# Kernel optimization log

Hardware: AMD Instinct MI355X
Metric: run time of the kernel (lower is better)

The kernel has to match this reference:

```python
import jax, jax.numpy as jnp
import numpy as np

B, Cin, C, H, W = 2, 64, 128, 64, 64
D_INNER, N_STATE, DT_RANK, K = 256, 16, 8, 4


def _silu(x):
    return x * jax.nn.sigmoid(x)


def _layernorm(x, g, b, eps=1e-5):
    mu = x.mean(-1, keepdims=True)
    var = ((x - mu) ** 2).mean(-1, keepdims=True)
    return (x - mu) * jax.lax.rsqrt(var + eps) * g + b


def setup_inputs():
    key = jax.random.key(0)
    ks = jax.random.split(key, 16)
    f32 = jnp.float32
    inp = {}
    inp["x"] = jax.random.normal(ks[0], (B, Cin, H, W), f32)
    inp["convin_w"] = jax.random.normal(ks[1], (C, Cin), f32) * 0.05
    inp["convin_b"] = jnp.zeros((C,), f32)
    inp["ln_g"] = jnp.ones((C,), f32)
    inp["ln_b"] = jnp.zeros((C,), f32)
    inp["in_proj_w"] = jax.random.normal(ks[2], (2 * D_INNER, C), f32) * 0.05
    inp["conv_w"] = jax.random.normal(ks[3], (D_INNER, 1, 3, 3), f32) * 0.1
    inp["conv_b"] = jnp.zeros((D_INNER,), f32)
    inp["x_proj_w"] = jax.random.normal(ks[4], (K, DT_RANK + 2 * N_STATE, D_INNER), f32) * 0.05
    inp["dt_w"] = jax.random.normal(ks[5], (K, D_INNER, DT_RANK), f32) * 0.1
    inp["dt_b"] = jax.random.uniform(ks[6], (K, D_INNER), f32, -4.0, -1.0)
    inp["A_logs"] = jnp.log(jnp.tile(jnp.arange(1, N_STATE + 1, dtype=f32), (K, D_INNER, 1)))
    inp["Ds"] = jnp.ones((K, D_INNER), f32)
    inp["outnorm_g"] = jnp.ones((D_INNER,), f32)
    inp["outnorm_b"] = jnp.zeros((D_INNER,), f32)
    inp["out_proj_w"] = jax.random.normal(ks[7], (C, D_INNER), f32) * 0.05
    inp["ca_fc1_w"] = jax.random.normal(ks[8], (C // 16, C), f32) * 0.1
    inp["ca_fc2_w"] = jax.random.normal(ks[9], (C, C // 16), f32) * 0.1
    inp["gn_g"] = jnp.ones((C,), f32)
    inp["gn_b"] = jnp.zeros((C,), f32)
    return inp


def _selective_scan(u, delta, A, Bm, Cm, Ds):
    # u, delta: (B,K,d,L); A: (K,d,N); Bm, Cm: (B,K,N,L); Ds: (K,d)
    def step(h, inp):
        u_t, dt, B_t, C_t = inp
        dA = jnp.exp(dt[..., None] * A)                      # (B,K,d,N)
        h = h * dA + dt[..., None] * B_t[:, :, None, :] * u_t[..., None]
        y = jnp.einsum('bkdn,bkn->bkd', h, C_t)
        return h, y
    step = jax.checkpoint(step)
    seq = (jnp.moveaxis(u, -1, 0), jnp.moveaxis(delta, -1, 0),
           jnp.moveaxis(Bm, -1, 0), jnp.moveaxis(Cm, -1, 0))
    h0 = jnp.zeros(u.shape[:3] + (A.shape[-1],), u.dtype)
    _, ys = jax.lax.scan(step, h0, seq)                      # (L,B,K,d)
    y = jnp.moveaxis(ys, 0, -1)                              # (B,K,d,L)
    return y + u * Ds[None, :, :, None]


def reference(x, convin_w, convin_b, ln_g, ln_b, in_proj_w, conv_w, conv_b,
              x_proj_w, dt_w, dt_b, A_logs, Ds, outnorm_g, outnorm_b,
              out_proj_w, ca_fc1_w, ca_fc2_w, gn_g, gn_b):
    L = H * W
    # 1x1 conv in
    x1 = jnp.einsum('bchw,oc->bohw', x, convin_w) + convin_b[None, :, None, None]
    m = x1.transpose(0, 2, 3, 1)                             # (B,H,W,C)
    # VSSBlock: LN -> SS2D -> residual
    m_ln = _layernorm(m, ln_g, ln_b)
    xz = m_ln @ in_proj_w.T                                  # (B,H,W,2*d_inner)
    xm, z = jnp.split(xz, 2, axis=-1)
    xm = xm.transpose(0, 3, 1, 2)                            # (B,d,H,W)
    xm = jax.lax.conv_general_dilated(xm, conv_w, (1, 1), [(1, 1), (1, 1)],
                                      feature_group_count=D_INNER)
    xm = _silu(xm + conv_b[None, :, None, None])
    x_flat = xm.reshape(B, D_INNER, L)
    x_tr = xm.transpose(0, 1, 3, 2).reshape(B, D_INNER, L)
    xs = jnp.stack([x_flat, x_tr, jnp.flip(x_flat, -1), jnp.flip(x_tr, -1)], axis=1)
    x_dbl = jnp.einsum('bkdl,kcd->bkcl', xs, x_proj_w)
    dts, Bs, Cs = jnp.split(x_dbl, [DT_RANK, DT_RANK + N_STATE], axis=2)
    delta = jax.nn.softplus(jnp.einsum('bkrl,kdr->bkdl', dts, dt_w) + dt_b[None, :, :, None])
    A = -jnp.exp(A_logs)                                     # (K,d,N)
    out_y = _selective_scan(xs, delta, A, Bs, Cs, Ds)        # (B,4,d,L)
    y0 = out_y[:, 0]
    y1 = out_y[:, 1].reshape(B, D_INNER, W, H).transpose(0, 1, 3, 2).reshape(B, D_INNER, L)
    y2 = jnp.flip(out_y[:, 2], -1)
    y3 = jnp.flip(out_y[:, 3], -1).reshape(B, D_INNER, W, H).transpose(0, 1, 3, 2).reshape(B, D_INNER, L)
    y = (y0 + y1 + y2 + y3).transpose(0, 2, 1).reshape(B, H, W, D_INNER)
    y = _layernorm(y, outnorm_g, outnorm_b)
    y = y * _silu(z)
    m_out = m + y @ out_proj_w.T                             # (B,H,W,C)
    mamba = m_out.transpose(0, 3, 1, 2)                      # (B,C,H,W)
    # CBAM-style channel attention
    def mlp(v):
        return jax.nn.relu(v @ ca_fc1_w.T) @ ca_fc2_w.T
    avg = mamba.mean((2, 3))
    mx = mamba.max((2, 3))
    att = jax.nn.sigmoid(mlp(avg) + mlp(mx))[:, :, None, None]
    ca = mamba * att
    # GroupNorm(2 groups) + SiLU + residual
    g = ca.reshape(B, 2, -1)
    mu = g.mean(-1, keepdims=True)
    var = ((g - mu) ** 2).mean(-1, keepdims=True)
    g = ((g - mu) * jax.lax.rsqrt(var + 1e-5)).reshape(B, C, H, W)
    g = g * gn_g[None, :, None, None] + gn_b[None, :, None, None]
    return _silu(g) + x1
```

## Files before the change

### kernel.cpp

```cpp
#include <hip/hip_runtime.h>
#include <math.h>


#define DEV __device__ __forceinline__

DEV float sigm_(float x){ return 1.f/(1.f+__expf(-x)); }
DEV float silu_(float x){ return x*sigm_(x); }
DEV float sp_(float x){ return (x>15.f)? x : __logf(1.f+__expf(x)); }

DEV int pos_dir(int k, int l){
  switch(k&3){
    case 0: return l;
    case 1: return ((l&63)<<6)|(l>>6);
    case 2: return 4095-l;
    default:{ int m=4095-l; return ((m&63)<<6)|(m>>6); }
  }
}

#define MM4x4(av,bv) do{ \
  acc[0][0]=fmaf(av.x,bv.x,acc[0][0]); acc[0][1]=fmaf(av.x,bv.y,acc[0][1]); \
  acc[0][2]=fmaf(av.x,bv.z,acc[0][2]); acc[0][3]=fmaf(av.x,bv.w,acc[0][3]); \
  acc[1][0]=fmaf(av.y,bv.x,acc[1][0]); acc[1][1]=fmaf(av.y,bv.y,acc[1][1]); \
  acc[1][2]=fmaf(av.y,bv.z,acc[1][2]); acc[1][3]=fmaf(av.y,bv.w,acc[1][3]); \
  acc[2][0]=fmaf(av.z,bv.x,acc[2][0]); acc[2][1]=fmaf(av.z,bv.y,acc[2][1]); \
  acc[2][2]=fmaf(av.z,bv.z,acc[2][2]); acc[2][3]=fmaf(av.z,bv.w,acc[2][3]); \
  acc[3][0]=fmaf(av.w,bv.x,acc[3][0]); acc[3][1]=fmaf(av.w,bv.y,acc[3][1]); \
  acc[3][2]=fmaf(av.w,bv.z,acc[3][2]); acc[3][3]=fmaf(av.w,bv.w,acc[3][3]); \
}while(0)

__global__ __launch_bounds__(256) void k_x1(const float* __restrict__ x,
    const float* __restrict__ W, const float* __restrict__ bias, float* __restrict__ x1){
  const int b = blockIdx.z;
  const int m0 = blockIdx.y*64, n0 = blockIdx.x*64;
  __shared__ float As[16][68], Bs[16][68];
  const int tid = threadIdx.x, tx = tid&15, ty = tid>>4;
  float acc[4][4]={};
  const float* Bb = x + (size_t)b*64*4096;
  for (int k0=0;k0<64;k0+=16){
    for (int i=tid;i<64*16;i+=256){ int m=i>>4,k=i&15; As[k][m]=W[(m0+m)*64+(k0+k)]; }
    for (int i=tid;i<16*64;i+=256){ int k=i>>6,n=i&63; Bs[k][n]=Bb[(size_t)(k0+k)*4096+(n0+n)]; }
    __syncthreads();
    #pragma unroll
    for (int k=0;k<16;++k){
      float4 av=*(const float4*)&As[k][ty*4];
      float4 bv=*(const float4*)&Bs[k][tx*4];
      MM4x4(av,bv);
    }
    __syncthreads();
  }
  #pragma unroll
  for (int i=0;i<4;++i){
    int o=m0+ty*4+i; float bs=bias[o];
    float4 v=make_float4(acc[i][0]+bs,acc[i][1]+bs,acc[i][2]+bs,acc[i][3]+bs);
    *(float4*)&x1[(size_t)((b<<7)+o)*4096 + n0+tx*4]=v;
  }
}

__global__ __launch_bounds__(256) void k_ln(const float* __restrict__ x1,
    const float* __restrict__ g, const float* __restrict__ be, float* __restrict__ mln){
  const int b=blockIdx.y, p0=blockIdx.x*32;
  __shared__ float tile[128][33];
  __shared__ float red[2][8][32];
  __shared__ float mean_s[32], rstd_s[32];
  const int tid=threadIdx.x;
  for (int i=tid;i<128*32;i+=256){ int o=i>>5,pp=i&31; tile[o][pp]=x1[(size_t)((b<<7)+o)*4096+p0+pp]; }
  __syncthreads();
  {
    int p=tid&31, seg=tid>>5;
    float s=0.f,s2=0.f;
    #pragma unroll
    for (int j=0;j<16;++j){ float v=tile[seg*16+j][p]; s+=v; s2=fmaf(v,v,s2); }
    red[0][seg][p]=s; red[1][seg][p]=s2;
  }
  __syncthreads();
  if (tid<32){
    float ss=0.f,ss2=0.f;
    #pragma unroll
    for (int sg=0;sg<8;++sg){ ss+=red[0][sg][tid]; ss2+=red[1][sg][tid]; }
    float mu=ss*(1.f/128.f), var=ss2*(1.f/128.f)-mu*mu;
    mean_s[tid]=mu; rstd_s[tid]=rsqrtf(var+1e-5f);
  }
  __syncthreads();
  for (int i=tid;i<128*32;i+=256){
    int o=i&127, pp=i>>7;
    float v=(tile[o][pp]-mean_s[pp])*rstd_s[pp]*g[o]+be[o];
    mln[(size_t)(b*4096+p0+pp)*128+o]=v;
  }
}

__global__ __launch_bounds__(256) void k_inproj(const float* __restrict__ mln,
    const float* __restrict__ W, float* __restrict__ xmpre_t, float* __restrict__ z){
  const int m0=blockIdx.y*64, n0=blockIdx.x*64;
  __shared__ float As[16][68], Bs[16][68];
  const int tid=threadIdx.x, tx=tid&15, ty=tid>>4;
  float acc[4][4]={};
  for (int k0=0;k0<128;k0+=16){
    for (int i=tid;i<64*16;i+=256){ int m=i>>4,k=i&15; As[k][m]=mln[(size_t)(m0+m)*128+(k0+k)]; }
    for (int i=tid;i<64*16;i+=256){ int n=i>>4,k=i&15; Bs[k][n]=W[(size_t)(n0+n)*128+(k0+k)]; }
    __syncthreads();
    #pragma unroll
    for (int k=0;k<16;++k){
      float4 av=*(const float4*)&As[k][ty*4];
      float4 bv=*(const float4*)&Bs[k][tx*4];
      MM4x4(av,bv);
    }
    __syncthreads();
  }
  const int col=n0+tx*4;
  #pragma unroll
  for (int i=0;i<4;++i){
    int row=m0+ty*4+i;
    float4 v=make_float4(acc[i][0],acc[i][1],acc[i][2],acc[i][3]);
    if (col<256) *(float4*)&xmpre_t[(size_t)row*256+col]=v;
    else         *(float4*)&z[(size_t)row*256+(col-256)]=v;
  }
}

__global__ __launch_bounds__(256) void k_dwconv(const float* __restrict__ xmpre_t,
    const float* __restrict__ cw, const float* __restrict__ cb, float* __restrict__ xflat_t){
  __shared__ float sw[2304];
  __shared__ float sb[256];
  const int tid=threadIdx.x;
  for (int i=tid;i<2304;i+=256) sw[i]=cw[i];
  sb[tid]=cb[tid];
  __syncthreads();
  const int bp0=blockIdx.x*16;
  const int b=bp0>>12, p0=bp0&4095;
  const int dq=tid&63, pg=tid>>6;
  const int d0=dq*4;
  float wr[9][4];
  #pragma unroll
  for (int t=0;t<9;++t)
    #pragma unroll
    for (int c=0;c<4;++c) wr[t][c]=sw[(d0+c)*9+t];
  const float4 bias=make_float4(sb[d0],sb[d0+1],sb[d0+2],sb[d0+3]);
  #pragma unroll
  for (int j=0;j<4;++j){
    const int p=p0+pg*4+j;
    const int h=p>>6, w=p&63;
    float4 acc=bias;
    #pragma unroll
    for (int dh=-1;dh<=1;++dh){
      int hh=h+dh; if ((unsigned)hh>=64u) continue;
      #pragma unroll
      for (int dw=-1;dw<=1;++dw){
        int ww=w+dw; if ((unsigned)ww>=64u) continue;
        const int t=(dh+1)*3+(dw+1);
        float4 iv=*(const float4*)&xmpre_t[((size_t)((b<<12)+hh*64+ww))*256+d0];
        acc.x=fmaf(iv.x,wr[t][0],acc.x); acc.y=fmaf(iv.y,wr[t][1],acc.y);
        acc.z=fmaf(iv.z,wr[t][2],acc.z); acc.w=fmaf(iv.w,wr[t][3],acc.w);
      }
    }
    acc.x=silu_(acc.x); acc.y=silu_(acc.y); acc.z=silu_(acc.z); acc.w=silu_(acc.w);
    *(float4*)&xflat_t[((size_t)((b<<12)+p))*256+d0]=acc;
  }
}

__global__ __launch_bounds__(256) void k_proj(const float* __restrict__ xflat_t,
    const float* __restrict__ xpw, float* __restrict__ pdt, float* __restrict__ pbc){
  const int b=blockIdx.z, n0=blockIdx.y*32, m0=blockIdx.x*64;
  __shared__ float As[16][68], Bs[16][36];
  const int tid=threadIdx.x, tx=tid&15, ty=tid>>4;
  float acc[4][2]={};
  for (int k0=0;k0<256;k0+=16){
    for (int i=tid;i<64*16;i+=256){ int m=i>>4,kk=i&15; As[kk][m]=xflat_t[((size_t)((b<<12)+m0+m))*256+k0+kk]; }
    for (int i=tid;i<32*16;i+=256){ int n=i>>4,kk=i&15; Bs[kk][n]=xpw[(size_t)(n0+n)*256+k0+kk]; }
    __syncthreads();
    #pragma unroll
    for (int kk=0;kk<16;++kk){
      float4 av=*(const float4*)&As[kk][ty*4];
      float2 bv=*(const float2*)&Bs[kk][tx*2];
      acc[0][0]=fmaf(av.x,bv.x,acc[0][0]); acc[0][1]=fmaf(av.x,bv.y,acc[0][1]);
      acc[1][0]=fmaf(av.y,bv.x,acc[1][0]); acc[1][1]=fmaf(av.y,bv.y,acc[1][1]);
      acc[2][0]=fmaf(av.z,bv.x,acc[2][0]); acc[2][1]=fmaf(av.z,bv.y,acc[2][1]);
      acc[3][0]=fmaf(av.w,bv.x,acc[3][0]); acc[3][1]=fmaf(av.w,bv.y,acc[3][1]);
    }
    __syncthreads();
  }
  #pragma unroll
  for (int i=0;i<4;++i){
    int l=m0+ty*4+i;
    #pragma unroll
    for (int j=0;j<2;++j){
      int r=n0+tx*2+j, kd=r/40, c=r%40, bk=b*4+kd;
      float v=acc[i][j];
      if (c<8) pdt[((size_t)bk*4096+l)*8+c]=v;
      else     pbc[((size_t)bk*4096+l)*32+(c-8)]=v;
    }
  }
}

__global__ __launch_bounds__(256) void k_scanA(const float* __restrict__ pdt,
    const float* __restrict__ pbc, const float* __restrict__ xflat_t,
    const float* __restrict__ dtw, const float* __restrict__ dtb,
    const float* __restrict__ A_logs, float* __restrict__ Pc, float* __restrict__ He){
  const int bx=blockIdx.x;
  const int ch=bx&127, k=(bx>>7)&3, b=bx>>9, bk=b*4+k;
  const int d=threadIdx.x;
  __shared__ float sbc[1024];
  __shared__ float sdt[256];
  for (int i=d;i<1024;i+=256) sbc[i]=pbc[((size_t)bk*4096+(ch<<5))*32+i];
  sdt[d]=pdt[((size_t)bk*4096+(ch<<5))*8+d];
  float acoef[16];
  const float* ap=&A_logs[((k<<8)+d)<<4];
  #pragma unroll
  for (int n=0;n<16;++n) acoef[n]=-__expf(ap[n]);
  bool pw=true;
  #pragma unroll
  for (int n=1;n<16;++n) pw = pw && (fabsf(acoef[n]-(float)(n+1)*acoef[0]) <= 1e-4f*fabsf(acoef[n]));
  float w8[8];
  {
    float4 w0=*(const float4*)&dtw[(size_t)k*2048+d*8];
    float4 w1=*(const float4*)&dtw[(size_t)k*2048+d*8+4];
    w8[0]=w0.x;w8[1]=w0.y;w8[2]=w0.z;w8[3]=w0.w;w8[4]=w1.x;w8[5]=w1.y;w8[6]=w1.z;w8[7]=w1.w;
  }
  const float dtbd=dtb[(k<<8)+d];
  __syncthreads();
  float h[16]; float sdv=0.f;
  #pragma unroll
  for (int n=0;n<16;++n) h[n]=0.f;
  const float* up=xflat_t+((size_t)b<<12)*256+d;
  if (pw){
    const float ac0=acoef[0];
    for (int s=0;s<32;++s){
      const int l=(ch<<5)+s;
      float t=dtbd;
      #pragma unroll
      for (int r=0;r<8;++r) t=fmaf(sdt[s*8+r],w8[r],t);
      const float dv=sp_(t);
      const float u=up[(size_t)pos_dir(k,l)*256];
      const float dvu=dv*u;
      sdv+=dv;
      const float e1=__expf(dv*ac0);
      float an=e1;
      h[0]=fmaf(h[0],an,dvu*sbc[s*32]);
      #pragma unroll
      for (int n=1;n<16;++n){ an*=e1; h[n]=fmaf(h[n],an,dvu*sbc[s*32+n]); }
    }
  } else {
    for (int s=0;s<32;++s){
      const int l=(ch<<5)+s;
      float t=dtbd;
      #pragma unroll
      for (int r=0;r<8;++r) t=fmaf(sdt[s*8+r],w8[r],t);
      const float dv=sp_(t);
      const float u=up[(size_t)pos_dir(k,l)*256];
      const float dvu=dv*u;
      sdv+=dv;
      #pragma unroll
      for (int n=0;n<16;++n){
        float a=__expf(dv*acoef[n]);
        h[n]=fmaf(h[n],a,dvu*sbc[s*32+n]);
      }
    }
  }
  const size_t obase=(size_t)ch*32768 + ((size_t)bk*256+d)*16;
  #pragma unroll
  for (int n=0;n<16;++n){ Pc[obase+n]=__expf(acoef[n]*sdv); He[obase+n]=h[n]; }
}

__global__ __launch_bounds__(256) void k_scanB(const float* __restrict__ Pc,
    const float* __restrict__ He, float* __restrict__ Hin){
  const int g=threadIdx.x&63, tc=threadIdx.x>>6;
  const int gid=blockIdx.x*64+g;
  float p[32], e[32];
  #pragma unroll
  for (int i=0;i<32;++i){
    size_t idx=(size_t)(tc*32+i)*32768+gid;
    p[i]=Pc[idx]; e[i]=He[idx];
  }
  float P=1.f, E=0.f;
  #pragma unroll
  for (int i=0;i<32;++i){ E=fmaf(E,p[i],e[i]); P*=p[i]; }
  __shared__ float sP[4][64], sE[4][64];
  sP[tc][g]=P; sE[tc][g]=E;
  __syncthreads();
  float Hp=0.f;
  for (int t=0;t<tc;++t) Hp=fmaf(Hp,sP[t][g],sE[t][g]);
  #pragma unroll
  for (int i=0;i<32;++i){
    Hin[(size_t)(tc*32+i)*32768+gid]=Hp;
    Hp=fmaf(Hp,p[i],e[i]);
  }
}

__global__ __launch_bounds__(256) void k_scanC(const float* __restrict__ pdt,
    const float* __restrict__ pbc, const float* __restrict__ xflat_t,
    const float* __restrict__ dtw, const float* __restrict__ dtb,
    const float* __restrict__ A_logs, const float* __restrict__ Ds,
    const float* __restrict__ Hin, float* __restrict__ y4){
  const int bx=blockIdx.x;
  const int ch=bx&127, k=(bx>>7)&3, b=bx>>9, bk=b*4+k;
  const int d=threadIdx.x;
  __shared__ float sbc[1024];
  __shared__ float sdt[256];
  for (int i=d;i<1024;i+=256) sbc[i]=pbc[((size_t)bk*4096+(ch<<5))*32+i];
  sdt[d]=pdt[((size_t)bk*4096+(ch<<5))*8+d];
  float acoef[16];
  const float* ap=&A_logs[((k<<8)+d)<<4];
  #pragma unroll
  for (int n=0;n<16;++n) acoef[n]=-__expf(ap[n]);
  bool pw=true;
  #pragma unroll
  for (int n=1;n<16;++n) pw = pw && (fabsf(acoef[n]-(float)(n+1)*acoef[0]) <= 1e-4f*fabsf(acoef[n]));
  float w8[8];
  {
    float4 w0=*(const float4*)&dtw[(size_t)k*2048+d*8];
    float4 w1=*(const float4*)&dtw[(size_t)k*2048+d*8+4];
    w8[0]=w0.x;w8[1]=w0.y;w8[2]=w0.z;w8[3]=w0.w;w8[4]=w1.x;w8[5]=w1.y;w8[6]=w1.z;w8[7]=w1.w;
  }
  const float dtbd=dtb[(k<<8)+d];
  const float dsv=Ds[(k<<8)+d];
  __syncthreads();
  const size_t ibase=(size_t)ch*32768 + ((size_t)bk*256+d)*16;
  float h[16];
  #pragma unroll
  for (int n=0;n<16;++n) h[n]=Hin[ibase+n];
  const float* up=xflat_t+((size_t)b<<12)*256+d;
  if (pw){
    const float ac0=acoef[0];
    for (int s=0;s<32;++s){
      const int l=(ch<<5)+s;
      float t=dtbd;
      #pragma unroll
      for (int r=0;r<8;++r) t=fmaf(sdt[s*8+r],w8[r],t);
      const float dv=sp_(t);
      const int pos=pos_dir(k,l);
      const float u=up[(size_t)pos*256];
      const float dvu=dv*u;
      const float e1=__expf(dv*ac0);
      float an=e1;
      float yv[16];
      h[0]=fmaf(h[0],an,dvu*sbc[s*32]);
      yv[0]=h[0]*sbc[s*32+16];
      #pragma unroll
      for (int n=1;n<16;++n){
        an*=e1;
        h[n]=fmaf(h[n],an,dvu*sbc[s*32+n]);
        yv[n]=h[n]*sbc[s*32+16+n];
      }
      #pragma unroll
      for (int st=8;st>0;st>>=1)
        #pragma unroll
        for (int n=0;n<st;++n) yv[n]+=yv[n+st];
      y4[((size_t)((b<<12)+pos)*4+k)*256+d]=yv[0]+u*dsv;
    }
  } else {
    for (int s=0;s<32;++s){
      const int l=(ch<<5)+s;
      float t=dtbd;
      #pragma unroll
      for (int r=0;r<8;++r) t=fmaf(sdt[s*8+r],w8[r],t);
      const float dv=sp_(t);
      const int pos=pos_dir(k,l);
      const float u=up[(size_t)pos*256];
      const float dvu=dv*u;
      float yv[16];
      #pragma unroll
      for (int n=0;n<16;++n){
        float a=__expf(dv*acoef[n]);
        h[n]=fmaf(h[n],a,dvu*sbc[s*32+n]);
        yv[n]=h[n]*sbc[s*32+16+n];
      }
      #pragma unroll
      for (int st=8;st>0;st>>=1)
        #pragma unroll
        for (int n=0;n<st;++n) yv[n]+=yv[n+st];
      y4[((size_t)((b<<12)+pos)*4+k)*256+d]=yv[0]+u*dsv;
    }
  }
}

__global__ __launch_bounds__(256) void k_outnorm(const float* __restrict__ y4,
    const float* __restrict__ g, const float* __restrict__ be,
    const float* __restrict__ z, float* __restrict__ yg){
  const int bp=blockIdx.x, d=threadIdx.x;
  const float* base=y4+(size_t)bp*1024;
  float v=base[d]+base[256+d]+base[512+d]+base[768+d];
  float s=v, s2=v*v;
  #pragma unroll
  for (int m=1;m<64;m<<=1){ s+=__shfl_xor(s,m); s2+=__shfl_xor(s2,m); }
  __shared__ float rs[4], rs2[4];
  if ((d&63)==0){ rs[d>>6]=s; rs2[d>>6]=s2; }
  __syncthreads();
  float S=rs[0]+rs[1]+rs[2]+rs[3], S2=rs2[0]+rs2[1]+rs2[2]+rs2[3];
  float mu=S*(1.f/256.f), var=S2*(1.f/256.f)-mu*mu, rstd=rsqrtf(var+1e-5f);
  float ln=(v-mu)*rstd*g[d]+be[d];
  float zv=z[(size_t)bp*256+d];
  yg[(size_t)bp*256+d]=ln*silu_(zv);
}

__global__ __launch_bounds__(256) void k_outproj(const float* __restrict__ yg,
    const float* __restrict__ W, const float* __restrict__ x1, float* __restrict__ mamba){
  const int b=blockIdx.z, m0=blockIdx.y*64, n0=blockIdx.x*64;
  __shared__ float As[16][68], Bs[16][68];
  const int tid=threadIdx.x, tx=tid&15, ty=tid>>4;
  float acc[4][4]={};
  const float* Yb=yg+(size_t)(b<<12)*256;
  for (int k0=0;k0<256;k0+=16){
    for (int i=tid;i<64*16;i+=256){ int m=i>>4,k=i&15; As[k][m]=W[(size_t)(m0+m)*256+(k0+k)]; }
    for (int i=tid;i<64*16;i+=256){ int n=i>>4,k=i&15; Bs[k][n]=Yb[(size_t)(n0+n)*256+(k0+k)]; }
    __syncthreads();
    #pragma unroll
    for (int k=0;k<16;++k){
      float4 av=*(const float4*)&As[k][ty*4];
      float4 bv=*(const float4*)&Bs[k][tx*4];
      MM4x4(av,bv);
    }
    __syncthreads();
  }
  #pragma unroll
  for (int i=0;i<4;++i){
    int c=m0+ty*4+i;
    size_t base=(size_t)((b<<7)+c)*4096 + n0+tx*4;
    float4 xv=*(const float4*)&x1[base];
    float4 v=make_float4(acc[i][0]+xv.x,acc[i][1]+xv.y,acc[i][2]+xv.z,acc[i][3]+xv.w);
    *(float4*)&mamba[base]=v;
  }
}

__global__ __launch_bounds__(256) void k_stats(const float* __restrict__ mamba, float* __restrict__ stats){
  const int bc=blockIdx.x, tid=threadIdx.x;
  const float* row=mamba+(size_t)bc*4096;
  float s=0.f,s2=0.f,mx=-3.402823466e38f;
  for (int i=tid;i<4096;i+=256){ float v=row[i]; s+=v; s2=fmaf(v,v,s2); mx=fmaxf(mx,v); }
  #pragma unroll
  for (int m=1;m<64;m<<=1){
    s+=__shfl_xor(s,m); s2+=__shfl_xor(s2,m); mx=fmaxf(mx,__shfl_xor(mx,m));
  }
  __shared__ float r0[4],r1[4],r2[4];
  if ((tid&63)==0){ int wv=tid>>6; r0[wv]=s; r1[wv]=s2; r2[wv]=mx; }
  __syncthreads();
  if (tid==0){
    stats[bc*3+0]=r0[0]+r0[1]+r0[2]+r0[3];
    stats[bc*3+1]=r1[0]+r1[1]+r1[2]+r1[3];
    stats[bc*3+2]=fmaxf(fmaxf(r2[0],r2[1]),fmaxf(r2[2],r2[3]));
  }
}

__global__ __launch_bounds__(256) void k_att(const float* __restrict__ stats,
    const float* __restrict__ fc1, const float* __restrict__ fc2,
    float* __restrict__ att, float* __restrict__ gstat){
  __shared__ float avg[2][128], mxs[2][128], S1[2][128], S2[2][128], hsum[2][8], attv[2][128];
  const int tid=threadIdx.x, b=tid>>7, c=tid&127;
  float s1=stats[tid*3], s2=stats[tid*3+1], m=stats[tid*3+2];
  avg[b][c]=s1*(1.f/4096.f); mxs[b][c]=m; S1[b][c]=s1; S2[b][c]=s2;
  __syncthreads();
  if (tid<16){
    int bb=tid>>3, i=tid&7;
    float ha=0.f,hm=0.f;
    for (int cc=0;cc<128;++cc){ float w=fc1[i*128+cc]; ha=fmaf(w,avg[bb][cc],ha); hm=fmaf(w,mxs[bb][cc],hm); }
    hsum[bb][i]=fmaxf(ha,0.f)+fmaxf(hm,0.f);
  }
  __syncthreads();
  float sacc=0.f;
  #pragma unroll
  for (int i=0;i<8;++i) sacc=fmaf(fc2[c*8+i],hsum[b][i],sacc);
  float a=sigm_(sacc);
  attv[b][c]=a; att[tid]=a;
  __syncthreads();
  if (tid<4){
    int bb=tid>>1, gp=tid&1;
    float sum1=0.f,sum2=0.f;
    for (int cc=0;cc<64;++cc){
      int c2=gp*64+cc; float av=attv[bb][c2];
      sum1=fmaf(av,S1[bb][c2],sum1);
      sum2=fmaf(av*av,S2[bb][c2],sum2);
    }
    const float inv=1.f/(64.f*4096.f);
    float mu=sum1*inv, ex2=sum2*inv, var=ex2-mu*mu;
    gstat[tid*2]=mu; gstat[tid*2+1]=rsqrtf(var+1e-5f);
  }
}

__global__ __launch_bounds__(256) void k_final(const float* __restrict__ mamba,
    const float* __restrict__ x1, const float* __restrict__ att,
    const float* __restrict__ gstat, const float* __restrict__ gg,
    const float* __restrict__ gb, float* __restrict__ out){
  const int idx=blockIdx.x*256+threadIdx.x;
  const int c=(idx>>12)&127, b=idx>>19;
  const int grp=(b<<1)+(c>>6);
  float v=mamba[idx]*att[(b<<7)+c];
  float vn=(v-gstat[grp*2])*gstat[grp*2+1]*gg[c]+gb[c];
  out[idx]=silu_(vn)+x1[idx];
}

extern "C" void kernel_launch(void* const* d_in, const int* in_sizes, int n_in,
                              void* d_out, int out_size, void* d_ws, size_t ws_size,
                              hipStream_t stream){
  (void)in_sizes; (void)n_in; (void)out_size; (void)ws_size;
  const float* x        =(const float*)d_in[0];
  const float* convin_w =(const float*)d_in[1];
  const float* convin_b =(const float*)d_in[2];
  const float* ln_g     =(const float*)d_in[3];
  const float* ln_b     =(const float*)d_in[4];
  const float* in_proj_w=(const float*)d_in[5];
  const float* conv_w   =(const float*)d_in[6];
  const float* conv_b   =(const float*)d_in[7];
  const float* x_proj_w =(const float*)d_in[8];
  const float* dt_w     =(const float*)d_in[9];
  const float* dt_b     =(const float*)d_in[10];
  const float* A_logs   =(const float*)d_in[11];
  const float* Ds       =(const float*)d_in[12];
  const float* outnorm_g=(const float*)d_in[13];
  const float* outnorm_b=(const float*)d_in[14];
  const float* out_proj_w=(const float*)d_in[15];
  const float* ca_fc1_w =(const float*)d_in[16];
  const float* ca_fc2_w =(const float*)d_in[17];
  const float* gn_g     =(const float*)d_in[18];
  const float* gn_b     =(const float*)d_in[19];

  float* ws=(float*)d_ws;
  size_t off=0;
  auto alloc=[&](size_t nfloats)->float*{ float* p=ws+off; off+=(nfloats+63)&~(size_t)63; return p; };
  float* x1     =alloc(1048576);
  float* mln    =alloc(1048576);
  float* z      =alloc(2097152);
  float* xmpre_t=alloc(2097152);
  float* xflat_t=alloc(2097152);
  float* pdt    =alloc(262144);
  float* pbc    =alloc(1048576);
  float* Pc     =alloc(4194304);
  float* He     =alloc(4194304);
  float* Hin    =alloc(4194304);
  float* y4     =alloc(8388608);
  float* yg     =alloc(2097152);
  float* mamba  =alloc(1048576);
  float* stats  =alloc(768);
  float* att    =alloc(256);
  float* gstat  =alloc(64);

  const dim3 blk(256);
  k_x1     <<<dim3(64,2,2), blk,0,stream>>>(x, convin_w, convin_b, x1);
  k_ln     <<<dim3(128,2),  blk,0,stream>>>(x1, ln_g, ln_b, mln);
  k_inproj <<<dim3(8,128),  blk,0,stream>>>(mln, in_proj_w, xmpre_t, z);
  k_dwconv <<<dim3(512),    blk,0,stream>>>(xmpre_t, conv_w, conv_b, xflat_t);
  k_proj   <<<dim3(64,5,2), blk,0,stream>>>(xflat_t, x_proj_w, pdt, pbc);
  k_scanA  <<<dim3(1024),   blk,0,stream>>>(pdt, pbc, xflat_t, dt_w, dt_b, A_logs, Pc, He);
  k_scanB  <<<dim3(512),    blk,0,stream>>>(Pc, He, Hin);
  k_scanC  <<<dim3(1024),   blk,0,stream>>>(pdt, pbc, xflat_t, dt_w, dt_b, A_logs, Ds, Hin, y4);
  k_outnorm<<<dim3(8192),   blk,0,stream>>>(y4, outnorm_g, outnorm_b, z, yg);
  k_outproj<<<dim3(64,2,2), blk,0,stream>>>(yg, out_proj_w, x1, mamba);
  k_stats  <<<dim3(256),    blk,0,stream>>>(mamba, stats);
  k_att    <<<dim3(1),      blk,0,stream>>>(stats, ca_fc1_w, ca_fc2_w, att, gstat);
  k_final  <<<dim3(4096),   blk,0,stream>>>(mamba, x1, att, gstat, gn_g, gn_b, (float*)d_out);
}
```

Before: 303.5 us.

## Emit local scan outputs in pass A and add carry-in correction in pass C

The chunked selective scan now writes each chunk's local output (zero initial state) during the first pass. The third pass only adds the contribution of the carried-in state, decayed by the cumulative delta, using just the C coefficients, so it no longer recomputes the full recurrence or re-reads the input. The first chunk's blocks exit early. The conv-in GEMM and LayerNorm are fused into one kernel, and workspace buffers are aliased, with scanB writing Hin in place over Pc. The risks are an extra read-modify-write of y4, a different rounding order in the closed-form decay, and the in-place aliasing, which relies on each scanB thread reading all its Pc values before writing.

New measurement: 301.7 us. No clear change (-0.6%).

```diff
diff --git a/kernel.cpp b/kernel.cpp
--- a/kernel.cpp
+++ b/kernel.cpp
@@ -28,64 +28,72 @@
   acc[3][2]=fmaf(av.w,bv.z,acc[3][2]); acc[3][3]=fmaf(av.w,bv.w,acc[3][3]); \
 }while(0)
 
-__global__ __launch_bounds__(256) void k_x1(const float* __restrict__ x,
-    const float* __restrict__ W, const float* __restrict__ bias, float* __restrict__ x1){
-  const int b = blockIdx.z;
-  const int m0 = blockIdx.y*64, n0 = blockIdx.x*64;
-  __shared__ float As[16][68], Bs[16][68];
-  const int tid = threadIdx.x, tx = tid&15, ty = tid>>4;
-  float acc[4][4]={};
-  const float* Bb = x + (size_t)b*64*4096;
-  for (int k0=0;k0<64;k0+=16){
-    for (int i=tid;i<64*16;i+=256){ int m=i>>4,k=i&15; As[k][m]=W[(m0+m)*64+(k0+k)]; }
-    for (int i=tid;i<16*64;i+=256){ int k=i>>6,n=i&63; Bs[k][n]=Bb[(size_t)(k0+k)*4096+(n0+n)]; }
-    __syncthreads();
-    #pragma unroll
-    for (int k=0;k<16;++k){
-      float4 av=*(const float4*)&As[k][ty*4];
-      float4 bv=*(const float4*)&Bs[k][tx*4];
-      MM4x4(av,bv);
-    }
-    __syncthreads();
-  }
-  #pragma unroll
-  for (int i=0;i<4;++i){
-    int o=m0+ty*4+i; float bs=bias[o];
-    float4 v=make_float4(acc[i][0]+bs,acc[i][1]+bs,acc[i][2]+bs,acc[i][3]+bs);
-    *(float4*)&x1[(size_t)((b<<7)+o)*4096 + n0+tx*4]=v;
-  }
-}
-
-__global__ __launch_bounds__(256) void k_ln(const float* __restrict__ x1,
-    const float* __restrict__ g, const float* __restrict__ be, float* __restrict__ mln){
-  const int b=blockIdx.y, p0=blockIdx.x*32;
-  __shared__ float tile[128][33];
-  __shared__ float red[2][8][32];
-  __shared__ float mean_s[32], rstd_s[32];
-  const int tid=threadIdx.x;
-  for (int i=tid;i<128*32;i+=256){ int o=i>>5,pp=i&31; tile[o][pp]=x1[(size_t)((b<<7)+o)*4096+p0+pp]; }
-  __syncthreads();
+__global__ __launch_bounds__(256) void k_x1ln(const float* __restrict__ x,
+    const float* __restrict__ W, const float* __restrict__ bias,
+    const float* __restrict__ g, const float* __restrict__ be,
+    float* __restrict__ x1, float* __restrict__ mln){
+  const int b=blockIdx.y, p0=blockIdx.x*64;
+  __shared__ float sw[64*132];
+  __shared__ float sx[64*68];
+  __shared__ float red[2][16][68];
+  __shared__ float smu[64], srs[64];
+  const int tid=threadIdx.x, tx=tid&15, ty=tid>>4;
+  for (int i=tid;i<8192;i+=256){ int c=i&63,o=i>>6; sw[c*132+o]=W[o*64+c]; }
+  for (int i=tid;i<4096;i+=256){ int c=i>>6,p=i&63; sx[c*68+p]=x[((size_t)(b*64+c))*4096+p0+p]; }
+  __syncthreads();
+  float acc[8][4]={};
+  for (int c=0;c<64;++c){
+    float4 a0=*(const float4*)&sw[c*132+ty*8];
+    float4 a1=*(const float4*)&sw[c*132+ty*8+4];
+    float4 bv=*(const float4*)&sx[c*68+tx*4];
+    acc[0][0]=fmaf(a0.x,bv.x,acc[0][0]); acc[0][1]=fmaf(a0.x,bv.y,acc[0][1]); acc[0][2]=fmaf(a0.x,bv.z,acc[0][2]); acc[0][3]=fmaf(a0.x,bv.w,acc[0][3]);
+    acc[1][0]=fmaf(a0.y,bv.x,acc[1][0]); acc[1][1]=fmaf(a0.y,bv.y,acc[1][1]); acc[1][2]=fmaf(a0.y,bv.z,acc[1][2]); acc[1][3]=fmaf(a0.y,bv.w,acc[1][3]);
+    acc[2][0]=fmaf(a0.z,bv.x,acc[2][0]); acc[2][1]=fmaf(a0.z,bv.y,acc[2][1]); acc[2][2]=fmaf(a0.z,bv.z,acc[2][2]); acc[2][3]=fmaf(a0.z,bv.w,acc[2][3]);
+    acc[3][0]=fmaf(a0.w,bv.x,acc[3][0]); acc[3][1]=fmaf(a0.w,bv.y,acc[3][1]); acc[3][2]=fmaf(a0.w,bv.z,acc[3][2]); acc[3][3]=fmaf(a0.w,bv.w,acc[3][3]);
+    acc[4][0]=fmaf(a1.x,bv.x,acc[4][0]); acc[4][1]=fmaf(a1.x,bv.y,acc[4][1]); acc[4][2]=fmaf(a1.x,bv.z,acc[4][2]); acc[4][3]=fmaf(a1.x,bv.w,acc[4][3]);
+    acc[5][0]=fmaf(a1.y,bv.x,acc[5][0]); acc[5][1]=fmaf(a1.y,bv.y,acc[5][1]); acc[5][2]=fmaf(a1.y,bv.z,acc[5][2]); acc[5][3]=fmaf(a1.y,bv.w,acc[5][3]);
+    acc[6][0]=fmaf(a1.z,bv.x,acc[6][0]); acc[6][1]=fmaf(a1.z,bv.y,acc[6][1]); acc[6][2]=fmaf(a1.z,bv.z,acc[6][2]); acc[6][3]=fmaf(a1.z,bv.w,acc[6][3]);
+    acc[7][0]=fmaf(a1.w,bv.x,acc[7][0]); acc[7][1]=fmaf(a1.w,bv.y,acc[7][1]); acc[7][2]=fmaf(a1.w,bv.z,acc[7][2]); acc[7][3]=fmaf(a1.w,bv.w,acc[7][3]);
+  }
+  float xr[8][4];
+  #pragma unroll
+  for (int i=0;i<8;++i){
+    float bs=bias[ty*8+i];
+    #pragma unroll
+    for (int j=0;j<4;++j) xr[i][j]=acc[i][j]+bs;
+  }
   {
-    int p=tid&31, seg=tid>>5;
-    float s=0.f,s2=0.f;
-    #pragma unroll
-    for (int j=0;j<16;++j){ float v=tile[seg*16+j][p]; s+=v; s2=fmaf(v,v,s2); }
-    red[0][seg][p]=s; red[1][seg][p]=s2;
-  }
-  __syncthreads();
-  if (tid<32){
-    float ss=0.f,ss2=0.f;
-    #pragma unroll
-    for (int sg=0;sg<8;++sg){ ss+=red[0][sg][tid]; ss2+=red[1][sg][tid]; }
-    float mu=ss*(1.f/128.f), var=ss2*(1.f/128.f)-mu*mu;
-    mean_s[tid]=mu; rstd_s[tid]=rsqrtf(var+1e-5f);
-  }
-  __syncthreads();
-  for (int i=tid;i<128*32;i+=256){
-    int o=i&127, pp=i>>7;
-    float v=(tile[o][pp]-mean_s[pp])*rstd_s[pp]*g[o]+be[o];
-    mln[(size_t)(b*4096+p0+pp)*128+o]=v;
-  }
+    float s[4]={},s2[4]={};
+    #pragma unroll
+    for (int i=0;i<8;++i)
+      #pragma unroll
+      for (int j=0;j<4;++j){ s[j]+=xr[i][j]; s2[j]=fmaf(xr[i][j],xr[i][j],s2[j]); }
+    #pragma unroll
+    for (int j=0;j<4;++j){ red[0][ty][tx*4+j]=s[j]; red[1][ty][tx*4+j]=s2[j]; }
+  }
+  __syncthreads();
+  if (tid<64){
+    float S=0.f,S2=0.f;
+    #pragma unroll
+    for (int t=0;t<16;++t){ S+=red[0][t][tid]; S2+=red[1][t][tid]; }
+    float mu=S*(1.f/128.f), var=S2*(1.f/128.f)-mu*mu;
+    smu[tid]=mu; srs[tid]=rsqrtf(var+1e-5f);
+  }
+  __syncthreads();
+  float* lnt=sw;
+  #pragma unroll
+  for (int i=0;i<8;++i){
+    int o=ty*8+i;
+    float gv=g[o], bev=be[o];
+    #pragma unroll
+    for (int j=0;j<4;++j){
+      int p=tx*4+j;
+      lnt[o*66+p]=(xr[i][j]-smu[p])*srs[p]*gv+bev;
+    }
+    *(float4*)&x1[((size_t)(b*128+o))*4096+p0+tx*4]=make_float4(xr[i][0],xr[i][1],xr[i][2],xr[i][3]);
+  }
+  __syncthreads();
+  for (int i=tid;i<8192;i+=256){ int p=i>>7,o=i&127; mln[((size_t)(b*4096+p0+p))*128+o]=lnt[o*66+p]; }
 }
 
 __global__ __launch_bounds__(256) void k_inproj(const float* __restrict__ mln,
@@ -193,7 +201,8 @@
 __global__ __launch_bounds__(256) void k_scanA(const float* __restrict__ pdt,
     const float* __restrict__ pbc, const float* __restrict__ xflat_t,
     const float* __restrict__ dtw, const float* __restrict__ dtb,
-    const float* __restrict__ A_logs, float* __restrict__ Pc, float* __restrict__ He){
+    const float* __restrict__ A_logs, const float* __restrict__ Ds,
+    float* __restrict__ Pc, float* __restrict__ He, float* __restrict__ y4){
   const int bx=blockIdx.x;
   const int ch=bx&127, k=(bx>>7)&3, b=bx>>9, bk=b*4+k;
   const int d=threadIdx.x;
@@ -201,13 +210,11 @@
   __shared__ float sdt[256];
   for (int i=d;i<1024;i+=256) sbc[i]=pbc[((size_t)bk*4096+(ch<<5))*32+i];
   sdt[d]=pdt[((size_t)bk*4096+(ch<<5))*8+d];
-  float acoef[16];
   const float* ap=&A_logs[((k<<8)+d)<<4];
-  #pragma unroll
-  for (int n=0;n<16;++n) acoef[n]=-__expf(ap[n]);
+  const float ac0=-__expf(ap[0]);
   bool pw=true;
   #pragma unroll
-  for (int n=1;n<16;++n) pw = pw && (fabsf(acoef[n]-(float)(n+1)*acoef[0]) <= 1e-4f*fabsf(acoef[n]));
+  for (int n=1;n<16;++n){ float an_=-__expf(ap[n]); pw=pw&&(fabsf(an_-(float)(n+1)*ac0)<=1e-4f*fabsf(an_)); }
   float w8[8];
   {
     float4 w0=*(const float4*)&dtw[(size_t)k*2048+d*8];
@@ -215,13 +222,13 @@
     w8[0]=w0.x;w8[1]=w0.y;w8[2]=w0.z;w8[3]=w0.w;w8[4]=w1.x;w8[5]=w1.y;w8[6]=w1.z;w8[7]=w1.w;
   }
   const float dtbd=dtb[(k<<8)+d];
+  const float dsv=Ds[(k<<8)+d];
   __syncthreads();
   float h[16]; float sdv=0.f;
   #pragma unroll
   for (int n=0;n<16;++n) h[n]=0.f;
   const float* up=xflat_t+((size_t)b<<12)*256+d;
   if (pw){
-    const float ac0=acoef[0];
     for (int s=0;s<32;++s){
       const int l=(ch<<5)+s;
       float t=dtbd;
@@ -231,13 +238,23 @@
       const float u=up[(size_t)pos_dir(k,l)*256];
       const float dvu=dv*u;
       sdv+=dv;
-      const float e1=__expf(dv*ac0);
-      float an=e1;
-      h[0]=fmaf(h[0],an,dvu*sbc[s*32]);
-      #pragma unroll
-      for (int n=1;n<16;++n){ an*=e1; h[n]=fmaf(h[n],an,dvu*sbc[s*32+n]); }
+      const float q=__expf(dv*ac0);
+      float an=q, yl=0.f;
+      #pragma unroll
+      for (int n4=0;n4<4;++n4){
+        float4 bb=*(const float4*)&sbc[s*32+n4*4];
+        float4 cc=*(const float4*)&sbc[s*32+16+n4*4];
+        h[n4*4+0]=fmaf(h[n4*4+0],an,dvu*bb.x); yl=fmaf(h[n4*4+0],cc.x,yl); an*=q;
+        h[n4*4+1]=fmaf(h[n4*4+1],an,dvu*bb.y); yl=fmaf(h[n4*4+1],cc.y,yl); an*=q;
+        h[n4*4+2]=fmaf(h[n4*4+2],an,dvu*bb.z); yl=fmaf(h[n4*4+2],cc.z,yl); an*=q;
+        h[n4*4+3]=fmaf(h[n4*4+3],an,dvu*bb.w); yl=fmaf(h[n4*4+3],cc.w,yl); an*=q;
+      }
+      y4[((size_t)((b<<12)+pos_dir(k,l))*4+k)*256+d]=yl+u*dsv;
     }
   } else {
+    float acoef[16];
+    #pragma unroll
+    for (int n=0;n<16;++n) acoef[n]=-__expf(ap[n]);
     for (int s=0;s<32;++s){
       const int l=(ch<<5)+s;
       float t=dtbd;
@@ -247,22 +264,35 @@
       const float u=up[(size_t)pos_dir(k,l)*256];
       const float dvu=dv*u;
       sdv+=dv;
+      float yl=0.f;
       #pragma unroll
       for (int n=0;n<16;++n){
         float a=__expf(dv*acoef[n]);
         h[n]=fmaf(h[n],a,dvu*sbc[s*32+n]);
+        yl=fmaf(h[n],sbc[s*32+16+n],yl);
       }
+      y4[((size_t)((b<<12)+pos_dir(k,l))*4+k)*256+d]=yl+u*dsv;
     }
   }
   const size_t obase=(size_t)ch*32768 + ((size_t)bk*256+d)*16;
-  #pragma unroll
-  for (int n=0;n<16;++n){ Pc[obase+n]=__expf(acoef[n]*sdv); He[obase+n]=h[n]; }
-}
-
-__global__ __launch_bounds__(256) void k_scanB(const float* __restrict__ Pc,
-    const float* __restrict__ He, float* __restrict__ Hin){
-  const int g=threadIdx.x&63, tc=threadIdx.x>>6;
-  const int gid=blockIdx.x*64+g;
+  if (pw){
+    const float qe=__expf(ac0*sdv);
+    float an=qe, pcv[16];
+    #pragma unroll
+    for (int n=0;n<16;++n){ pcv[n]=an; an*=qe; }
+    #pragma unroll
+    for (int n4=0;n4<4;++n4) *(float4*)&Pc[obase+n4*4]=make_float4(pcv[n4*4],pcv[n4*4+1],pcv[n4*4+2],pcv[n4*4+3]);
+  } else {
+    #pragma unroll
+    for (int n=0;n<16;++n) Pc[obase+n]=__expf(-__expf(ap[n])*sdv);
+  }
+  #pragma unroll
+  for (int n4=0;n4<4;++n4) *(float4*)&He[obase+n4*4]=make_float4(h[n4*4],h[n4*4+1],h[n4*4+2],h[n4*4+3]);
+}
+
+__global__ __launch_bounds__(256) void k_scanB(const float* Pc, const float* He, float* Hin){
+  const int g2=threadIdx.x&63, tc=threadIdx.x>>6;
+  const int gid=blockIdx.x*64+g2;
   float p[32], e[32];
   #pragma unroll
   for (int i=0;i<32;++i){
@@ -273,10 +303,10 @@
   #pragma unroll
   for (int i=0;i<32;++i){ E=fmaf(E,p[i],e[i]); P*=p[i]; }
   __shared__ float sP[4][64], sE[4][64];
-  sP[tc][g]=P; sE[tc][g]=E;
+  sP[tc][g2]=P; sE[tc][g2]=E;
   __syncthreads();
   float Hp=0.f;
-  for (int t=0;t<tc;++t) Hp=fmaf(Hp,sP[t][g],sE[t][g]);
+  for (int t=0;t<tc;++t) Hp=fmaf(Hp,sP[t][g2],sE[t][g2]);
   #pragma unroll
   for (int i=0;i<32;++i){
     Hin[(size_t)(tc*32+i)*32768+gid]=Hp;
@@ -284,25 +314,23 @@
   }
 }
 
-__global__ __launch_bounds__(256) void k_scanC(const float* __restrict__ pdt,
-    const float* __restrict__ pbc, const float* __restrict__ xflat_t,
-    const float* __restrict__ dtw, const float* __restrict__ dtb,
-    const float* __restrict__ A_logs, const float* __restrict__ Ds,
+__global__ __launch_bounds__(256) void k_scanC2(const float* __restrict__ pdt,
+    const float* __restrict__ pbc, const float* __restrict__ dtw,
+    const float* __restrict__ dtb, const float* __restrict__ A_logs,
     const float* __restrict__ Hin, float* __restrict__ y4){
   const int bx=blockIdx.x;
   const int ch=bx&127, k=(bx>>7)&3, b=bx>>9, bk=b*4+k;
+  if (ch==0) return;
   const int d=threadIdx.x;
-  __shared__ float sbc[1024];
+  __shared__ float sC[512];
   __shared__ float sdt[256];
-  for (int i=d;i<1024;i+=256) sbc[i]=pbc[((size_t)bk*4096+(ch<<5))*32+i];
+  for (int i=d;i<512;i+=256){ int s=i>>4,n=i&15; sC[i]=pbc[((size_t)bk*4096+(ch<<5)+s)*32+16+n]; }
   sdt[d]=pdt[((size_t)bk*4096+(ch<<5))*8+d];
-  float acoef[16];
   const float* ap=&A_logs[((k<<8)+d)<<4];
-  #pragma unroll
-  for (int n=0;n<16;++n) acoef[n]=-__expf(ap[n]);
+  const float ac0=-__expf(ap[0]);
   bool pw=true;
   #pragma unroll
-  for (int n=1;n<16;++n) pw = pw && (fabsf(acoef[n]-(float)(n+1)*acoef[0]) <= 1e-4f*fabsf(acoef[n]));
+  for (int n=1;n<16;++n){ float an_=-__expf(ap[n]); pw=pw&&(fabsf(an_-(float)(n+1)*ac0)<=1e-4f*fabsf(an_)); }
   float w8[8];
   {
     float4 w0=*(const float4*)&dtw[(size_t)k*2048+d*8];
@@ -310,63 +338,49 @@
     w8[0]=w0.x;w8[1]=w0.y;w8[2]=w0.z;w8[3]=w0.w;w8[4]=w1.x;w8[5]=w1.y;w8[6]=w1.z;w8[7]=w1.w;
   }
   const float dtbd=dtb[(k<<8)+d];
-  const float dsv=Ds[(k<<8)+d];
   __syncthreads();
   const size_t ibase=(size_t)ch*32768 + ((size_t)bk*256+d)*16;
   float h[16];
   #pragma unroll
-  for (int n=0;n<16;++n) h[n]=Hin[ibase+n];
-  const float* up=xflat_t+((size_t)b<<12)*256+d;
+  for (int n4=0;n4<4;++n4){
+    float4 hv=*(const float4*)&Hin[ibase+n4*4];
+    h[n4*4]=hv.x; h[n4*4+1]=hv.y; h[n4*4+2]=hv.z; h[n4*4+3]=hv.w;
+  }
   if (pw){
-    const float ac0=acoef[0];
+    float cumd=0.f;
     for (int s=0;s<32;++s){
+      float t=dtbd;
+      #pragma unroll
+      for (int r=0;r<8;++r) t=fmaf(sdt[s*8+r],w8[r],t);
+      cumd+=sp_(t);
+      const float q=__expf(ac0*cumd);
+      float an=q, corr=0.f;
+      #pragma unroll
+      for (int n4=0;n4<4;++n4){
+        float4 cc=*(const float4*)&sC[s*16+n4*4];
+        corr=fmaf(h[n4*4+0]*an,cc.x,corr); an*=q;
+        corr=fmaf(h[n4*4+1]*an,cc.y,corr); an*=q;
+        corr=fmaf(h[n4*4+2]*an,cc.z,corr); an*=q;
+        corr=fmaf(h[n4*4+3]*an,cc.w,corr); an*=q;
+      }
       const int l=(ch<<5)+s;
+      y4[((size_t)((b<<12)+pos_dir(k,l))*4+k)*256+d]+=corr;
+    }
+  } else {
+    float acoef[16];
+    #pragma unroll
+    for (int n=0;n<16;++n) acoef[n]=-__expf(ap[n]);
+    float cumd=0.f;
+    for (int s=0;s<32;++s){
       float t=dtbd;
       #pragma unroll
       for (int r=0;r<8;++r) t=fmaf(sdt[s*8+r],w8[r],t);
-      const float dv=sp_(t);
-      const int pos=pos_dir(k,l);
-      const float u=up[(size_t)pos*256];
-      const float dvu=dv*u;
-      const float e1=__expf(dv*ac0);
-      float an=e1;
-      float yv[16];
-      h[0]=fmaf(h[0],an,dvu*sbc[s*32]);
-      yv[0]=h[0]*sbc[s*32+16];
-      #pragma unroll
-      for (int n=1;n<16;++n){
-        an*=e1;
-        h[n]=fmaf(h[n],an,dvu*sbc[s*32+n]);
-        yv[n]=h[n]*sbc[s*32+16+n];
-      }
-      #pragma unroll
-      for (int st=8;st>0;st>>=1)
-        #pragma unroll
-        for (int n=0;n<st;++n) yv[n]+=yv[n+st];
-      y4[((size_t)((b<<12)+pos)*4+k)*256+d]=yv[0]+u*dsv;
-    }
-  } else {
-    for (int s=0;s<32;++s){
+      cumd+=sp_(t);
+      float corr=0.f;
+      #pragma unroll
+      for (int n=0;n<16;++n) corr=fmaf(h[n]*__expf(acoef[n]*cumd),sC[s*16+n],corr);
       const int l=(ch<<5)+s;
-      float t=dtbd;
-      #pragma unroll
-      for (int r=0;r<8;++r) t=fmaf(sdt[s*8+r],w8[r],t);
-      const float dv=sp_(t);
-      const int pos=pos_dir(k,l);
-      const float u=up[(size_t)pos*256];
-      const float dvu=dv*u;
-      float yv[16];
-      #pragma unroll
-      for (int n=0;n<16;++n){
-        float a=__expf(dv*acoef[n]);
-        h[n]=fmaf(h[n],a,dvu*sbc[s*32+n]);
-        yv[n]=h[n]*sbc[s*32+16+n];
-      }
-      #pragma unroll
-      for (int st=8;st>0;st>>=1)
-        #pragma unroll
-        for (int n=0;n<st;++n) yv[n]+=yv[n+st];
-      y4[((size_t)((b<<12)+pos)*4+k)*256+d]=yv[0]+u*dsv;
+      y4[((size_t)((b<<12)+pos_dir(k,l))*4+k)*256+d]+=corr;
     }
   }
 }
@@ -511,34 +525,30 @@
   const float* gn_b     =(const float*)d_in[19];
 
   float* ws=(float*)d_ws;
-  size_t off=0;
-  auto alloc=[&](size_t nfloats)->float*{ float* p=ws+off; off+=(nfloats+63)&~(size_t)63; return p; };
-  float* x1     =alloc(1048576);
-  float* mln    =alloc(1048576);
-  float* z      =alloc(2097152);
-  float* xmpre_t=alloc(2097152);
-  float* xflat_t=alloc(2097152);
-  float* pdt    =alloc(262144);
-  float* pbc    =alloc(1048576);
-  float* Pc     =alloc(4194304);
-  float* He     =alloc(4194304);
-  float* Hin    =alloc(4194304);
-  float* y4     =alloc(8388608);
-  float* yg     =alloc(2097152);
-  float* mamba  =alloc(1048576);
-  float* stats  =alloc(768);
-  float* att    =alloc(256);
-  float* gstat  =alloc(64);
+  float* x1     =ws+0;
+  float* z      =ws+1048576;
+  float* xmpre_t=ws+3145728;
+  float* mln    =ws+5242880;
+  float* xflat_t=ws+6291456;
+  float* pdt    =ws+8388608;
+  float* pbc    =ws+8912896;
+  float* Pc     =ws+10485760;
+  float* He     =ws+14680064;
+  float* y4     =ws+18874368;
+  float* yg     =ws+3145728;
+  float* mamba  =ws+5242880;
+  float* stats  =ws+27262976;
+  float* att    =stats+768;
+  float* gstat  =att+256;
 
   const dim3 blk(256);
-  k_x1     <<<dim3(64,2,2), blk,0,stream>>>(x, convin_w, convin_b, x1);
-  k_ln     <<<dim3(128,2),  blk,0,stream>>>(x1, ln_g, ln_b, mln);
+  k_x1ln   <<<dim3(64,2),   blk,0,stream>>>(x, convin_w, convin_b, ln_g, ln_b, x1, mln);
   k_inproj <<<dim3(8,128),  blk,0,stream>>>(mln, in_proj_w, xmpre_t, z);
   k_dwconv <<<dim3(512),    blk,0,stream>>>(xmpre_t, conv_w, conv_b, xflat_t);
   k_proj   <<<dim3(64,5,2), blk,0,stream>>>(xflat_t, x_proj_w, pdt, pbc);
-  k_scanA  <<<dim3(1024),   blk,0,stream>>>(pdt, pbc, xflat_t, dt_w, dt_b, A_logs, Pc, He);
-  k_scanB  <<<dim3(512),    blk,0,stream>>>(Pc, He, Hin);
-  k_scanC  <<<dim3(1024),   blk,0,stream>>>(pdt, pbc, xflat_t, dt_w, dt_b, A_logs, Ds, Hin, y4);
+  k_scanA  <<<dim3(1024),   blk,0,stream>>>(pdt, pbc, xflat_t, dt_w, dt_b, A_logs, Ds, Pc, He, y4);
+  k_scanB  <<<dim3(512),    blk,0,stream>>>(Pc, He, Pc );
+  k_scanC2 <<<dim3(1024),   blk,0,stream>>>(pdt, pbc, dt_w, dt_b, A_logs, Pc , y4);
   k_outnorm<<<dim3(8192),   blk,0,stream>>>(y4, outnorm_g, outnorm_b, z, yg);
   k_outproj<<<dim3(64,2,2), blk,0,stream>>>(yg, out_proj_w, x1, mamba);
   k_stats  <<<dim3(256),    blk,0,stream>>>(mamba, stats);
```
